# Optimization experiments

Hardware: AMD Instinct MI355X
Metric: run time of the kernel (lower is better)

Reference implementation:

```python
import jax, jax.numpy as jnp
import numpy as np

# Dimensions (source globals scaled to production: r=256 residues, s=128 sequences)
S, R, CM, CZ, C, H = 128, 256, 256, 128, 32, 8
EPS = 1e-5  # torch LayerNorm default


def setup_inputs() -> dict:
    key = jax.random.key(0)
    ks = jax.random.split(key, 14)
    msa = jax.random.normal(ks[0], (S, R, CM), dtype=jnp.float32)
    pair = jax.random.normal(ks[1], (R, R, CZ), dtype=jnp.float32)
    u = lambda k, shape, fan: jax.random.uniform(k, shape, jnp.float32, -1.0 / np.sqrt(fan), 1.0 / np.sqrt(fan))
    return {
        "msa": msa,
        "pair": pair,
        # per-head LayerNorm affine params (stacked over head axis)
        "ln_msa_g": 1.0 + 0.1 * jax.random.normal(ks[2], (H, CM), dtype=jnp.float32),
        "ln_msa_b": 0.1 * jax.random.normal(ks[3], (H, CM), dtype=jnp.float32),
        "ln_pair_g": 1.0 + 0.1 * jax.random.normal(ks[4], (H, CZ), dtype=jnp.float32),
        "ln_pair_b": 0.1 * jax.random.normal(ks[5], (H, CZ), dtype=jnp.float32),
        # per-head projections (torch Linear without bias; stored as (in, out))
        "Wq": u(ks[6], (H, CM, C), CM),
        "Wk": u(ks[7], (H, CM, C), CM),
        "Wv": u(ks[8], (H, CM, C), CM),
        "Wg": u(ks[9], (H, CM, C), CM),
        "Wb": u(ks[10], (H, CZ, S), CZ),  # linear_b: c_z -> s
        # output projection c*H -> c_m (with bias)
        "Wo": u(ks[11], (H * C, CM), H * C),
        "bo": u(ks[12], (CM,), H * C),
    }


def _forward(msa, pair, ln_msa_g, ln_msa_b, ln_pair_g, ln_pair_b, Wq, Wk, Wv, Wg, Wb, Wo, bo):
    # LayerNorm normalization is head-independent; only affine differs per head.
    mu = msa.mean(-1, keepdims=True)
    var = msa.var(-1, keepdims=True)
    nm = (msa - mu) * jax.lax.rsqrt(var + EPS)              # (S, R, CM)
    p = nm[None] * ln_msa_g[:, None, None, :] + ln_msa_b[:, None, None, :]  # (H, S, R, CM)

    q = jnp.einsum("hsrc,hcd->hsrd", p, Wq)                  # (H, S, R, C)
    k = jnp.einsum("hsrc,hcd->hsrd", p, Wk)
    v = jnp.einsum("hsrc,hcd->hsrd", p, Wv)
    g = jax.nn.sigmoid(jnp.einsum("hsrc,hcd->hsrd", p, Wg))

    pmu = pair.mean(-1, keepdims=True)
    pvar = pair.var(-1, keepdims=True)
    npair = (pair - pmu) * jax.lax.rsqrt(pvar + EPS)         # (R, R, CZ)
    pp = npair[None] * ln_pair_g[:, None, None, :] + ln_pair_b[:, None, None, :]  # (H, R, R, CZ)
    bflat = jnp.einsum("hijc,hcs->hijs", pp, Wb)             # (H, R, R, S)
    # Faithful to torch: b = linear_b(flat_pair).view(s, r, r) -- a raw
    # row-major reinterpretation (NOT a transpose).
    b = bflat.reshape(H, S, R, R)

    inv_sqrt_c = np.float32(1.0 / np.sqrt(C))
    scores = (jnp.einsum("hsid,hsjd->hsij", q, k) + b) * inv_sqrt_c  # (H, S, R, R)
    # Source softmax is over dim=-2 (the query/row axis), faithful here.
    a = jax.nn.softmax(scores, axis=-2)
    o = g * jnp.einsum("hsij,hsjd->hsid", a, v)              # (H, S, R, C)

    # concat heads on last dim: (S, R, H*C)
    cat = jnp.transpose(o, (1, 2, 0, 3)).reshape(S, R, H * C)
    return cat @ Wo + bo                                      # (S, R, CM)


def reference(msa, pair, ln_msa_g, ln_msa_b, ln_pair_g, ln_pair_b, Wq, Wk, Wv, Wg, Wb, Wo, bo):
    return _forward(msa, pair, ln_msa_g, ln_msa_b, ln_pair_g, ln_pair_b, Wq, Wk, Wv, Wg, Wb, Wo, bo)
```

## Files before the change

kernel.cpp:

```cpp
#include <hip/hip_runtime.h>
#include <hip/hip_bf16.h>


namespace {
constexpr int S_ = 128, R_ = 256, CM_ = 256, CZ_ = 128, C_ = 32, H_ = 8;
constexpr int SR_ = S_ * R_;
constexpr int RR_ = R_ * R_;
constexpr float EPS_ = 1e-5f;
constexpr float ISC_ = 0.17677669529663687f;

constexpr size_t OFF_MU_M = 0;
constexpr size_t OFF_RS_M = OFF_MU_M + SR_;
constexpr size_t OFF_MU_P = OFF_RS_M + SR_;
constexpr size_t OFF_RS_P = OFF_MU_P + RR_;
constexpr size_t OFF_WC   = OFF_RS_P + RR_;
constexpr size_t OFF_BC   = OFF_WC + (size_t)H_ * CM_ * 128;
constexpr size_t OFF_WBP  = OFF_BC + (size_t)H_ * 128;
constexpr size_t OFF_BBP  = OFF_WBP + (size_t)H_ * CZ_ * 128;
constexpr size_t F32_END  = OFF_BBP + (size_t)H_ * 128;
constexpr size_t BF_BASE  = F32_END * 4;
constexpr size_t QKVG_ELEMS = (size_t)H_ * SR_ * C_;
constexpr size_t CAT_ELEMS  = (size_t)SR_ * CM_;
constexpr size_t WBT_ELEMS  = (size_t)H_ * 128 * 128;
constexpr size_t WOT_ELEMS  = (size_t)256 * 256;
constexpr size_t NEED_BYTES =
    BF_BASE + (4 * QKVG_ELEMS + CAT_ELEMS + WBT_ELEMS + WOT_ELEMS) * 2;
}

typedef unsigned short bf_t;
typedef short s8v __attribute__((ext_vector_type(8)));
typedef float f4v __attribute__((ext_vector_type(4)));

__device__ __forceinline__ unsigned pk2(float lo, float hi) {
  __hip_bfloat162 t = __float22bfloat162_rn(float2{lo, hi});
  return *reinterpret_cast<unsigned*>(&t);
}
__device__ __forceinline__ bf_t pk1(float v) {
  __hip_bfloat16 t = __float2bfloat16(v);
  return *reinterpret_cast<bf_t*>(&t);
}
__device__ __forceinline__ float uplo(unsigned u) { return __uint_as_float(u << 16); }
__device__ __forceinline__ float uphi(unsigned u) { return __uint_as_float(u & 0xffff0000u); }
__device__ __forceinline__ void up8(uint4 u, float* f) {
  f[0] = uplo(u.x); f[1] = uphi(u.x);
  f[2] = uplo(u.y); f[3] = uphi(u.y);
  f[4] = uplo(u.z); f[5] = uphi(u.z);
  f[6] = uplo(u.w); f[7] = uphi(u.w);
}
__device__ __forceinline__ f4v mfma16(s8v a, s8v b, f4v c) {
  return __builtin_amdgcn_mfma_f32_16x16x32_bf16(a, b, c, 0, 0, 0);
}

__global__ void msa_stats_k(const float* __restrict__ msa, float* __restrict__ mu,
                            float* __restrict__ rstd) {
  int row = blockIdx.x * 4 + (threadIdx.x >> 6);
  int lane = threadIdx.x & 63;
  float4 v = reinterpret_cast<const float4*>(msa + (size_t)row * CM_)[lane];
  float s = v.x + v.y + v.z + v.w;
  float s2 = v.x * v.x + v.y * v.y + v.z * v.z + v.w * v.w;
  for (int off = 32; off; off >>= 1) {
    s += __shfl_down(s, off);
    s2 += __shfl_down(s2, off);
  }
  if (lane == 0) {
    float m = s / CM_;
    float var = s2 / CM_ - m * m;
    mu[row] = m;
    rstd[row] = rsqrtf(var + EPS_);
  }
}

__global__ void pair_stats_k(const float* __restrict__ pair, float* __restrict__ mu,
                             float* __restrict__ rstd) {
  int row = blockIdx.x * 4 + (threadIdx.x >> 6);
  int lane = threadIdx.x & 63;
  float2 v = reinterpret_cast<const float2*>(pair + (size_t)row * CZ_)[lane];
  float s = v.x + v.y;
  float s2 = v.x * v.x + v.y * v.y;
  for (int off = 32; off; off >>= 1) {
    s += __shfl_down(s, off);
    s2 += __shfl_down(s2, off);
  }
  if (lane == 0) {
    float m = s / CZ_;
    float var = s2 / CZ_ - m * m;
    mu[row] = m;
    rstd[row] = rsqrtf(var + EPS_);
  }
}

__global__ void prep_weights_k(const float* __restrict__ lng_m, const float* __restrict__ lnb_m,
                               const float* __restrict__ lng_p, const float* __restrict__ lnb_p,
                               const float* __restrict__ Wq, const float* __restrict__ Wk,
                               const float* __restrict__ Wv, const float* __restrict__ Wg,
                               const float* __restrict__ Wb, const float* __restrict__ Wo,
                               bf_t* __restrict__ wct, float* __restrict__ bc,
                               float* __restrict__ Wbp, float* __restrict__ bbp,
                               bf_t* __restrict__ wbt, bf_t* __restrict__ wot) {
  int b = blockIdx.x;
  int t = threadIdx.x;
  if (b < H_) {
    int h = b;
    int m = t >> 5, d = t & 31;
    const float* Wsrc = (m == 0) ? Wq : (m == 1) ? Wk : (m == 2) ? Wv : Wg;
    float scale = (m == 0) ? ISC_ : 1.0f;
    float bias = 0.f;
    for (int c = 0; c < CM_; c++) {
      float w = Wsrc[((size_t)h * CM_ + c) * C_ + d];
      bias += lnb_m[h * CM_ + c] * w;
      wct[((size_t)h * 128 + t) * 256 + c] = pk1(lng_m[h * CM_ + c] * w * scale);
    }
    bc[h * 128 + t] = bias * scale;
  } else if (b < 2 * H_) {
    int h = b - H_;
    float bias = 0.f;
    for (int c = 0; c < CZ_; c++) {
      float w = Wb[((size_t)h * CZ_ + c) * S_ + t];
      bias += lnb_p[h * CZ_ + c] * w;
      Wbp[((size_t)h * CZ_ + c) * 128 + t] = lng_p[h * CZ_ + c] * w * ISC_;
    }
    bbp[h * 128 + t] = bias * ISC_;
    for (int c = 0; c < CZ_; c++)
      wbt[((size_t)h * 128 + t) * 128 + c] = pk1(Wbp[((size_t)h * CZ_ + c) * 128 + t]);
  } else {
    int n = (b - 2 * H_) * 128 + t;
    for (int k = 0; k < 256; k++) wot[(size_t)n * 256 + k] = pk1(Wo[(size_t)k * 256 + n]);
  }
}

__global__ __launch_bounds__(512, 1) void qkvg_mfma_k(
    const float* __restrict__ msa, const float* __restrict__ mu, const float* __restrict__ rstd,
    const bf_t* __restrict__ wct, const float* __restrict__ bc, bf_t* __restrict__ q,
    bf_t* __restrict__ k, bf_t* __restrict__ v, bf_t* __restrict__ g) {
  __shared__ bf_t sm_a[128 * 256];
  __shared__ bf_t sm_w[128 * 256];
  int ib = blockIdx.x;
  int tid = threadIdx.x;
  int w = tid >> 6, l = tid & 63;
  int l15 = l & 15, l4 = l >> 4;
  int iw = w >> 2, jw = w & 3;
  int sr0 = ib * 128;
  int sx7 = l15 & 7;
#pragma unroll
  for (int rep = 0; rep < 8; rep++) {
    int flat = rep * 512 + tid;
    int row = flat >> 5, c = flat & 31;
    int srow = sr0 + row;
    const float4* ps = reinterpret_cast<const float4*>(msa + (size_t)srow * CM_ + c * 8);
    float4 x0 = ps[0], x1 = ps[1];
    float m = mu[srow], rs = rstd[srow];
    uint4 wv;
    wv.x = pk2((x0.x - m) * rs, (x0.y - m) * rs);
    wv.y = pk2((x0.z - m) * rs, (x0.w - m) * rs);
    wv.z = pk2((x1.x - m) * rs, (x1.y - m) * rs);
    wv.w = pk2((x1.z - m) * rs, (x1.w - m) * rs);
    *reinterpret_cast<uint4*>(&sm_a[row * 256 + ((c ^ (row & 7)) << 3)]) = wv;
  }
  for (int h = 0; h < H_; h++) {
    __syncthreads();
#pragma unroll
    for (int rep = 0; rep < 8; rep++) {
      int flat = rep * 512 + tid;
      int row = flat >> 5, c = flat & 31;
      *reinterpret_cast<uint4*>(&sm_w[row * 256 + ((c ^ (row & 7)) << 3)]) =
          *reinterpret_cast<const uint4*>(wct + ((size_t)h * 128 + row) * 256 + c * 8);
    }
    f4v acc[4][2];
#pragma unroll
    for (int jt = 0; jt < 2; jt++) {
      float bb = bc[h * 128 + jw * 32 + jt * 16 + l15];
#pragma unroll
      for (int it = 0; it < 4; it++) acc[it][jt] = f4v{bb, bb, bb, bb};
    }
    __syncthreads();
#pragma unroll
    for (int ks = 0; ks < 8; ks++) {
      int ch = ks * 4 + l4;
      s8v a[4], b[2];
#pragma unroll
      for (int it = 0; it < 4; it++)
        a[it] = *reinterpret_cast<const s8v*>(
            &sm_a[(iw * 64 + it * 16 + l15) * 256 + ((ch ^ sx7) << 3)]);
#pragma unroll
      for (int jt = 0; jt < 2; jt++)
        b[jt] = *reinterpret_cast<const s8v*>(
            &sm_w[(jw * 32 + jt * 16 + l15) * 256 + ((ch ^ sx7) << 3)]);
#pragma unroll
      for (int it = 0; it < 4; it++)
#pragma unroll
        for (int jt = 0; jt < 2; jt++) acc[it][jt] = mfma16(a[it], b[jt], acc[it][jt]);
    }
#pragma unroll
    for (int it = 0; it < 4; it++) {
#pragma unroll
      for (int jt = 0; jt < 2; jt++) {
        int j = jw * 32 + jt * 16 + l15;
        int m_ = j >> 5, d = j & 31;
        bf_t* dst = (m_ == 0) ? q : (m_ == 1) ? k : (m_ == 2) ? v : g;
#pragma unroll
        for (int r = 0; r < 4; r++) {
          int i = iw * 64 + it * 16 + l4 * 4 + r;
          float val = acc[it][jt][r];
          if (m_ == 3) val = 1.f / (1.f + __expf(-val));
          dst[((size_t)h * SR_ + sr0 + i) * C_ + d] = pk1(val);
        }
      }
    }
  }
}

__global__ __launch_bounds__(512, 1) void attn_mfma_k(
    const float* __restrict__ pair, const float* __restrict__ mu_p,
    const float* __restrict__ rs_p, const bf_t* __restrict__ wbt,
    const float* __restrict__ bbp, const bf_t* __restrict__ qg, const bf_t* __restrict__ kg,
    const bf_t* __restrict__ vg, const bf_t* __restrict__ gg, bf_t* __restrict__ cat) {
  __shared__ bf_t sm_pN[256 * 128];
  __shared__ bf_t sm_wt[64 * 128];
  __shared__ bf_t sm_p[256 * 64];
  __shared__ bf_t sm_q[256 * 40];
  __shared__ bf_t sm_k[64 * 40];
  __shared__ bf_t sm_vt[32 * 64];
  __shared__ float sm_redm[4 * 64];
  __shared__ float sm_reds[4 * 64];

  int s = blockIdx.x, h = blockIdx.y;
  int tid = threadIdx.x;
  int w = tid >> 6, l = tid & 63;
  int l15 = l & 15, l4 = l >> 4;
  int iw = w >> 1, jw = w & 1;
  int iw2 = w >> 1, dw = w & 1;
  size_t base = ((size_t)h * SR_ + (size_t)s * R_) * C_;

#pragma unroll
  for (int rep = 0; rep < 2; rep++) {
    int flat = rep * 512 + tid;
    int row = flat >> 2, c = flat & 3;
    *reinterpret_cast<uint4*>(&sm_q[row * 40 + c * 8]) =
        *reinterpret_cast<const uint4*>(qg + base + (size_t)row * C_ + c * 8);
  }

  f4v accO[4];
#pragma unroll
  for (int it = 0; it < 4; it++) accO[it] = f4v{0.f, 0.f, 0.f, 0.f};

  for (int p = 0; p < 2; p++) {
    __syncthreads();
#pragma unroll
    for (int rep = 0; rep < 8; rep++) {
      int flat = rep * 512 + tid;
      int row = flat >> 4, c = flat & 15;
      int gr = (2 * s + (row >> 7)) * 256 + 2 * (row & 127) + p;
      const float4* ps = reinterpret_cast<const float4*>(pair + (size_t)gr * CZ_) + c * 2;
      float4 x0 = ps[0], x1 = ps[1];
      float m = mu_p[gr], rs = rs_p[gr];
      uint4 wv;
      wv.x = pk2((x0.x - m) * rs, (x0.y - m) * rs);
      wv.y = pk2((x0.z - m) * rs, (x0.w - m) * rs);
      wv.z = pk2((x1.x - m) * rs, (x1.y - m) * rs);
      wv.w = pk2((x1.z - m) * rs, (x1.w - m) * rs);
      *reinterpret_cast<uint4*>(&sm_pN[row * 128 + ((c ^ (row & 7)) << 3)]) = wv;
    }
    for (int jh = 0; jh < 2; jh++) {
      int j0 = p * 128 + jh * 64;
      __syncthreads();
#pragma unroll
      for (int rep = 0; rep < 2; rep++) {
        int flat = rep * 512 + tid;
        int row = flat >> 4, c = flat & 15;
        *reinterpret_cast<uint4*>(&sm_wt[row * 128 + ((c ^ (row & 7)) << 3)]) =
            *reinterpret_cast<const uint4*>(wbt + ((size_t)h * 128 + jh * 64 + row) * 128 +
                                            c * 8);
      }
      if (tid < 256) {
        int row = tid >> 2, c = tid & 3;
        *reinterpret_cast<uint4*>(&sm_k[row * 40 + c * 8]) =
            *reinterpret_cast<const uint4*>(kg + base + (size_t)(j0 + row) * C_ + c * 8);
      } else {
        int t2 = tid - 256;
        int j = t2 >> 2, dc = t2 & 3;
        uint4 u = *reinterpret_cast<const uint4*>(vg + base + (size_t)(j0 + j) * C_ + dc * 8);
        unsigned uu[4] = {u.x, u.y, u.z, u.w};
#pragma unroll
        for (int e = 0; e < 8; e++) {
          int d = dc * 8 + e;
          bf_t val = (bf_t)((uu[e >> 1] >> ((e & 1) * 16)) & 0xffff);
          sm_vt[d * 64 + ((((j >> 3) ^ (d & 7)) << 3) + (j & 7))] = val;
        }
      }
      f4v acc[4][2];
      {
        float bb0 = bbp[h * 128 + jh * 64 + jw * 32 + l15];
        float bb1 = bbp[h * 128 + jh * 64 + jw * 32 + 16 + l15];
#pragma unroll
        for (int it = 0; it < 4; it++) {
          acc[it][0] = f4v{bb0, bb0, bb0, bb0};
          acc[it][1] = f4v{bb1, bb1, bb1, bb1};
        }
      }
      __syncthreads();
      int sx7 = l15 & 7;
#pragma unroll
      for (int ks = 0; ks < 4; ks++) {
        int ch = (ks * 4 + l4);
        s8v a[4], b[2];
#pragma unroll
        for (int it = 0; it < 4; it++)
          a[it] = *reinterpret_cast<const s8v*>(
              &sm_pN[(iw * 64 + it * 16 + l15) * 128 + ((ch ^ sx7) << 3)]);
#pragma unroll
        for (int u = 0; u < 2; u++)
          b[u] = *reinterpret_cast<const s8v*>(
              &sm_wt[(jw * 32 + u * 16 + l15) * 128 + ((ch ^ sx7) << 3)]);
#pragma unroll
        for (int it = 0; it < 4; it++) {
          acc[it][0] = mfma16(a[it], b[0], acc[it][0]);
          acc[it][1] = mfma16(a[it], b[1], acc[it][1]);
        }
      }
      {
        s8v qa[4], kb[2];
#pragma unroll
        for (int it = 0; it < 4; it++)
          qa[it] = *reinterpret_cast<const s8v*>(&sm_q[(iw * 64 + it * 16 + l15) * 40 + l4 * 8]);
#pragma unroll
        for (int u = 0; u < 2; u++)
          kb[u] = *reinterpret_cast<const s8v*>(&sm_k[(jw * 32 + u * 16 + l15) * 40 + l4 * 8]);
#pragma unroll
        for (int it = 0; it < 4; it++) {
          acc[it][0] = mfma16(qa[it], kb[0], acc[it][0]);
          acc[it][1] = mfma16(qa[it], kb[1], acc[it][1]);
        }
      }
      float mx[2];
#pragma unroll
      for (int u = 0; u < 2; u++) {
        float m0 = -1e30f;
#pragma unroll
        for (int it = 0; it < 4; it++)
#pragma unroll
          for (int r = 0; r < 4; r++) m0 = fmaxf(m0, acc[it][u][r]);
        m0 = fmaxf(m0, __shfl_xor(m0, 16));
        m0 = fmaxf(m0, __shfl_xor(m0, 32));
        mx[u] = m0;
      }
      if (l < 16) {
        sm_redm[iw * 64 + jw * 32 + l] = mx[0];
        sm_redm[iw * 64 + jw * 32 + 16 + l] = mx[1];
      }
      __syncthreads();
      float M[2], sm[2];
#pragma unroll
      for (int u = 0; u < 2; u++) {
        int jc = jw * 32 + u * 16 + l15;
        float m0 = sm_redm[jc];
        m0 = fmaxf(m0, sm_redm[64 + jc]);
        m0 = fmaxf(m0, sm_redm[128 + jc]);
        m0 = fmaxf(m0, sm_redm[192 + jc]);
        M[u] = m0;
        float s0 = 0.f;
#pragma unroll
        for (int it = 0; it < 4; it++) {
#pragma unroll
          for (int r = 0; r < 4; r++) {
            float e = __expf(acc[it][u][r] - m0);
            acc[it][u][r] = e;
            s0 += e;
          }
        }
        s0 += __shfl_xor(s0, 16);
        s0 += __shfl_xor(s0, 32);
        sm[u] = s0;
      }
      if (l < 16) {
        sm_reds[iw * 64 + jw * 32 + l] = sm[0];
        sm_reds[iw * 64 + jw * 32 + 16 + l] = sm[1];
      }
      __syncthreads();
#pragma unroll
      for (int u = 0; u < 2; u++) {
        int jc = jw * 32 + u * 16 + l15;
        float tot = sm_reds[jc] + sm_reds[64 + jc] + sm_reds[128 + jc] + sm_reds[192 + jc];
        float inv = 1.0f / tot;
#pragma unroll
        for (int it = 0; it < 4; it++) {
#pragma unroll
          for (int r = 0; r < 4; r++) {
            int i = iw * 64 + it * 16 + l4 * 4 + r;
            sm_p[i * 64 + ((((jc >> 3) ^ (i & 7)) << 3) + (jc & 7))] = pk1(acc[it][u][r] * inv);
          }
        }
      }
      __syncthreads();
#pragma unroll
      for (int ks = 0; ks < 2; ks++) {
        int ch = ks * 4 + l4;
        s8v vb = *reinterpret_cast<const s8v*>(
            &sm_vt[(dw * 16 + l15) * 64 + ((ch ^ sx7) << 3)]);
#pragma unroll
        for (int it = 0; it < 4; it++) {
          s8v pa = *reinterpret_cast<const s8v*>(
              &sm_p[(iw2 * 64 + it * 16 + l15) * 64 + ((ch ^ sx7) << 3)]);
          accO[it] = mfma16(pa, vb, accO[it]);
        }
      }
    }
  }
#pragma unroll
  for (int it = 0; it < 4; it++) {
#pragma unroll
    for (int r = 0; r < 4; r++) {
      int i = iw2 * 64 + it * 16 + l4 * 4 + r;
      int d = dw * 16 + l15;
      float gf = uplo((unsigned)gg[base + (size_t)i * C_ + d]);
      cat[((size_t)s * R_ + i) * 256 + h * 32 + d] = pk1(accO[it][r] * gf);
    }
  }
}

__global__ __launch_bounds__(512, 1) void out_mfma_k(const bf_t* __restrict__ cat,
                                                     const bf_t* __restrict__ wot,
                                                     const float* __restrict__ bo,
                                                     float* __restrict__ out) {
  __shared__ bf_t sm_a[128 * 256];
  __shared__ bf_t sm_b[128 * 256];
  int ib = blockIdx.x;
  int tid = threadIdx.x;
  int w = tid >> 6, l = tid & 63;
  int l15 = l & 15, l4 = l >> 4, sx7 = l15 & 7;
  int iw = w >> 2, jw = w & 3;
  int sr0 = ib * 128;
#pragma unroll
  for (int rep = 0; rep < 8; rep++) {
    int flat = rep * 512 + tid;
    int row = flat >> 5, c = flat & 31;
    *reinterpret_cast<uint4*>(&sm_a[row * 256 + ((c ^ (row & 7)) << 3)]) =
        *reinterpret_cast<const uint4*>(cat + (size_t)(sr0 + row) * 256 + c * 8);
  }
  for (int nb = 0; nb < 2; nb++) {
    __syncthreads();
#pragma unroll
    for (int rep = 0; rep < 8; rep++) {
      int flat = rep * 512 + tid;
      int row = flat >> 5, c = flat & 31;
      *reinterpret_cast<uint4*>(&sm_b[row * 256 + ((c ^ (row & 7)) << 3)]) =
          *reinterpret_cast<const uint4*>(wot + (size_t)(nb * 128 + row) * 256 + c * 8);
    }
    f4v acc[4][2];
#pragma unroll
    for (int jt = 0; jt < 2; jt++) {
      float bb = bo[nb * 128 + jw * 32 + jt * 16 + l15];
#pragma unroll
      for (int it = 0; it < 4; it++) acc[it][jt] = f4v{bb, bb, bb, bb};
    }
    __syncthreads();
#pragma unroll
    for (int ks = 0; ks < 8; ks++) {
      int ch = ks * 4 + l4;
      s8v a[4], b[2];
#pragma unroll
      for (int it = 0; it < 4; it++)
        a[it] = *reinterpret_cast<const s8v*>(
            &sm_a[(iw * 64 + it * 16 + l15) * 256 + ((ch ^ sx7) << 3)]);
#pragma unroll
      for (int jt = 0; jt < 2; jt++)
        b[jt] = *reinterpret_cast<const s8v*>(
            &sm_b[(jw * 32 + jt * 16 + l15) * 256 + ((ch ^ sx7) << 3)]);
#pragma unroll
      for (int it = 0; it < 4; it++)
#pragma unroll
        for (int jt = 0; jt < 2; jt++) acc[it][jt] = mfma16(a[it], b[jt], acc[it][jt]);
    }
#pragma unroll
    for (int it = 0; it < 4; it++)
#pragma unroll
      for (int jt = 0; jt < 2; jt++) {
        int n = nb * 128 + jw * 32 + jt * 16 + l15;
#pragma unroll
        for (int r = 0; r < 4; r++) {
          int i = iw * 64 + it * 16 + l4 * 4 + r;
          out[(size_t)(sr0 + i) * 256 + n] = acc[it][jt][r];
        }
      }
  }
}

extern "C" void kernel_launch(void* const* d_in, const int* in_sizes, int n_in, void* d_out,
                              int out_size, void* d_ws, size_t ws_size, hipStream_t stream) {
  if (ws_size < NEED_BYTES) return;

  const float* msa = (const float*)d_in[0];
  const float* pair = (const float*)d_in[1];
  const float* lng_m = (const float*)d_in[2];
  const float* lnb_m = (const float*)d_in[3];
  const float* lng_p = (const float*)d_in[4];
  const float* lnb_p = (const float*)d_in[5];
  const float* Wq = (const float*)d_in[6];
  const float* Wk = (const float*)d_in[7];
  const float* Wv = (const float*)d_in[8];
  const float* Wg = (const float*)d_in[9];
  const float* Wb = (const float*)d_in[10];
  const float* Wo = (const float*)d_in[11];
  const float* bo = (const float*)d_in[12];
  float* out = (float*)d_out;
  float* ws = (float*)d_ws;

  float* mu_m = ws + OFF_MU_M;
  float* rs_m = ws + OFF_RS_M;
  float* mu_p = ws + OFF_MU_P;
  float* rs_p = ws + OFF_RS_P;
  bf_t* wct = (bf_t*)(ws + OFF_WC);
  float* bc = ws + OFF_BC;
  float* Wbp = ws + OFF_WBP;
  float* bbp = ws + OFF_BBP;
  bf_t* qb = (bf_t*)((char*)d_ws + BF_BASE);
  bf_t* kb = qb + QKVG_ELEMS;
  bf_t* vb = kb + QKVG_ELEMS;
  bf_t* gb = vb + QKVG_ELEMS;
  bf_t* cat = gb + QKVG_ELEMS;
  bf_t* wbt = cat + CAT_ELEMS;
  bf_t* wot = wbt + WBT_ELEMS;

  msa_stats_k<<<SR_ / 4, 256, 0, stream>>>(msa, mu_m, rs_m);
  pair_stats_k<<<RR_ / 4, 256, 0, stream>>>(pair, mu_p, rs_p);
  prep_weights_k<<<18, 128, 0, stream>>>(lng_m, lnb_m, lng_p, lnb_p, Wq, Wk, Wv, Wg, Wb, Wo, wct,
                                         bc, Wbp, bbp, wbt, wot);
  qkvg_mfma_k<<<SR_ / 128, 512, 0, stream>>>(msa, mu_m, rs_m, wct, bc, qb, kb, vb, gb);
  attn_mfma_k<<<dim3(S_, H_), 512, 0, stream>>>(pair, mu_p, rs_p, wbt, bbp, qb, kb, vb, gb, cat);
  out_mfma_k<<<SR_ / 128, 512, 0, stream>>>(cat, wot, bo, out);
}
```

Measured before the change: 182.5 us.

## Prenormalize pair to bf16, cut LDS staging, raise occupancy across MFMA kernels

The pair LayerNorm becomes a kernel that writes normalized bf16 rows to workspace, so attention no longer normalizes fp32 pair rows in each block. Attention, QKVG and output kernels drop most shared-memory staging: weights, pair rows, q and k are read straight from global/L2 into MFMA operands. GEMM tiles shrink to 64 rows with launch bounds allowing 4 blocks per CU, which doubles the grid and cuts LDS per block. The aim is higher occupancy and fewer barriers, at the cost of more redundant global/L2 traffic and unswizzled direct loads.

Result: slower. 362.7 us (+98.8%).

```diff
diff --git a/kernel.cpp b/kernel.cpp
--- a/kernel.cpp
+++ b/kernel.cpp
@@ -11,9 +11,7 @@
 
 constexpr size_t OFF_MU_M = 0;
 constexpr size_t OFF_RS_M = OFF_MU_M + SR_;
-constexpr size_t OFF_MU_P = OFF_RS_M + SR_;
-constexpr size_t OFF_RS_P = OFF_MU_P + RR_;
-constexpr size_t OFF_WC   = OFF_RS_P + RR_;
+constexpr size_t OFF_WC   = OFF_RS_M + SR_;
 constexpr size_t OFF_BC   = OFF_WC + (size_t)H_ * CM_ * 128;
 constexpr size_t OFF_WBP  = OFF_BC + (size_t)H_ * 128;
 constexpr size_t OFF_BBP  = OFF_WBP + (size_t)H_ * CZ_ * 128;
@@ -23,8 +21,9 @@
 constexpr size_t CAT_ELEMS  = (size_t)SR_ * CM_;
 constexpr size_t WBT_ELEMS  = (size_t)H_ * 128 * 128;
 constexpr size_t WOT_ELEMS  = (size_t)256 * 256;
+constexpr size_t PAIRN_ELEMS = (size_t)RR_ * 128;
 constexpr size_t NEED_BYTES =
-    BF_BASE + (4 * QKVG_ELEMS + CAT_ELEMS + WBT_ELEMS + WOT_ELEMS) * 2;
+    BF_BASE + (4 * QKVG_ELEMS + CAT_ELEMS + WBT_ELEMS + WOT_ELEMS + PAIRN_ELEMS) * 2;
 }
 
 typedef unsigned short bf_t;
@@ -41,14 +40,11 @@
 }
 __device__ __forceinline__ float uplo(unsigned u) { return __uint_as_float(u << 16); }
 __device__ __forceinline__ float uphi(unsigned u) { return __uint_as_float(u & 0xffff0000u); }
-__device__ __forceinline__ void up8(uint4 u, float* f) {
-  f[0] = uplo(u.x); f[1] = uphi(u.x);
-  f[2] = uplo(u.y); f[3] = uphi(u.y);
-  f[4] = uplo(u.z); f[5] = uphi(u.z);
-  f[6] = uplo(u.w); f[7] = uphi(u.w);
-}
 __device__ __forceinline__ f4v mfma16(s8v a, s8v b, f4v c) {
   return __builtin_amdgcn_mfma_f32_16x16x32_bf16(a, b, c, 0, 0, 0);
+}
+__device__ __forceinline__ s8v ld8(const bf_t* p) {
+  return *reinterpret_cast<const s8v*>(p);
 }
 
 __global__ void msa_stats_k(const float* __restrict__ msa, float* __restrict__ mu,
@@ -70,23 +66,22 @@
   }
 }
 
-__global__ void pair_stats_k(const float* __restrict__ pair, float* __restrict__ mu,
-                             float* __restrict__ rstd) {
-  int row = blockIdx.x * 4 + (threadIdx.x >> 6);
+__global__ __launch_bounds__(512) void pair_norm_k(const float* __restrict__ pair,
+                                                   bf_t* __restrict__ pairN) {
+  int row = blockIdx.x * 8 + (threadIdx.x >> 6);
   int lane = threadIdx.x & 63;
   float2 v = reinterpret_cast<const float2*>(pair + (size_t)row * CZ_)[lane];
   float s = v.x + v.y;
   float s2 = v.x * v.x + v.y * v.y;
   for (int off = 32; off; off >>= 1) {
-    s += __shfl_down(s, off);
-    s2 += __shfl_down(s2, off);
-  }
-  if (lane == 0) {
-    float m = s / CZ_;
-    float var = s2 / CZ_ - m * m;
-    mu[row] = m;
-    rstd[row] = rsqrtf(var + EPS_);
-  }
+    s += __shfl_xor(s, off);
+    s2 += __shfl_xor(s2, off);
+  }
+  float m = s / CZ_;
+  float var = s2 / CZ_ - m * m;
+  float rs = rsqrtf(var + EPS_);
+  reinterpret_cast<unsigned*>(pairN)[(size_t)row * 64 + lane] =
+      pk2((v.x - m) * rs, (v.y - m) * rs);
 }
 
 __global__ void prep_weights_k(const float* __restrict__ lng_m, const float* __restrict__ lnb_m,
@@ -128,21 +123,19 @@
   }
 }
 
-__global__ __launch_bounds__(512, 1) void qkvg_mfma_k(
+__global__ __launch_bounds__(512, 4) void qkvg_mfma_k(
     const float* __restrict__ msa, const float* __restrict__ mu, const float* __restrict__ rstd,
     const bf_t* __restrict__ wct, const float* __restrict__ bc, bf_t* __restrict__ q,
     bf_t* __restrict__ k, bf_t* __restrict__ v, bf_t* __restrict__ g) {
-  __shared__ bf_t sm_a[128 * 256];
-  __shared__ bf_t sm_w[128 * 256];
+  __shared__ bf_t sm_a[64 * 256];
   int ib = blockIdx.x;
   int tid = threadIdx.x;
   int w = tid >> 6, l = tid & 63;
-  int l15 = l & 15, l4 = l >> 4;
+  int l15 = l & 15, l4 = l >> 4, sx7 = l15 & 7;
   int iw = w >> 2, jw = w & 3;
-  int sr0 = ib * 128;
-  int sx7 = l15 & 7;
-#pragma unroll
-  for (int rep = 0; rep < 8; rep++) {
+  int sr0 = ib * 64;
+#pragma unroll
+  for (int rep = 0; rep < 4; rep++) {
     int flat = rep * 512 + tid;
     int row = flat >> 5, c = flat & 31;
     int srow = sr0 + row;
@@ -156,42 +149,32 @@
     wv.w = pk2((x1.z - m) * rs, (x1.w - m) * rs);
     *reinterpret_cast<uint4*>(&sm_a[row * 256 + ((c ^ (row & 7)) << 3)]) = wv;
   }
+  __syncthreads();
   for (int h = 0; h < H_; h++) {
-    __syncthreads();
-#pragma unroll
-    for (int rep = 0; rep < 8; rep++) {
-      int flat = rep * 512 + tid;
-      int row = flat >> 5, c = flat & 31;
-      *reinterpret_cast<uint4*>(&sm_w[row * 256 + ((c ^ (row & 7)) << 3)]) =
-          *reinterpret_cast<const uint4*>(wct + ((size_t)h * 128 + row) * 256 + c * 8);
-    }
-    f4v acc[4][2];
+    f4v acc[2][2];
 #pragma unroll
     for (int jt = 0; jt < 2; jt++) {
       float bb = bc[h * 128 + jw * 32 + jt * 16 + l15];
 #pragma unroll
-      for (int it = 0; it < 4; it++) acc[it][jt] = f4v{bb, bb, bb, bb};
-    }
-    __syncthreads();
+      for (int it = 0; it < 2; it++) acc[it][jt] = f4v{bb, bb, bb, bb};
+    }
 #pragma unroll
     for (int ks = 0; ks < 8; ks++) {
       int ch = ks * 4 + l4;
-      s8v a[4], b[2];
-#pragma unroll
-      for (int it = 0; it < 4; it++)
-        a[it] = *reinterpret_cast<const s8v*>(
-            &sm_a[(iw * 64 + it * 16 + l15) * 256 + ((ch ^ sx7) << 3)]);
+      s8v a[2], b[2];
+#pragma unroll
+      for (int it = 0; it < 2; it++)
+        a[it] = ld8(&sm_a[(iw * 32 + it * 16 + l15) * 256 + ((ch ^ sx7) << 3)]);
 #pragma unroll
       for (int jt = 0; jt < 2; jt++)
-        b[jt] = *reinterpret_cast<const s8v*>(
-            &sm_w[(jw * 32 + jt * 16 + l15) * 256 + ((ch ^ sx7) << 3)]);
-#pragma unroll
-      for (int it = 0; it < 4; it++)
+        b[jt] = ld8(&wct[((size_t)h * 128 + jw * 32 + jt * 16 + l15) * 256 + ch * 8]);
+#pragma unroll
+      for (int it = 0; it < 2; it++)
 #pragma unroll
         for (int jt = 0; jt < 2; jt++) acc[it][jt] = mfma16(a[it], b[jt], acc[it][jt]);
     }
 #pragma unroll
-    for (int it = 0; it < 4; it++) {
+    for (int it = 0; it < 2; it++) {
 #pragma unroll
       for (int jt = 0; jt < 2; jt++) {
         int j = jw * 32 + jt * 16 + l15;
@@ -199,7 +182,7 @@
         bf_t* dst = (m_ == 0) ? q : (m_ == 1) ? k : (m_ == 2) ? v : g;
 #pragma unroll
         for (int r = 0; r < 4; r++) {
-          int i = iw * 64 + it * 16 + l4 * 4 + r;
+          int i = iw * 32 + it * 16 + l4 * 4 + r;
           float val = acc[it][jt][r];
           if (m_ == 3) val = 1.f / (1.f + __expf(-val));
           dst[((size_t)h * SR_ + sr0 + i) * C_ + d] = pk1(val);
@@ -209,16 +192,11 @@
   }
 }
 
-__global__ __launch_bounds__(512, 1) void attn_mfma_k(
-    const float* __restrict__ pair, const float* __restrict__ mu_p,
-    const float* __restrict__ rs_p, const bf_t* __restrict__ wbt,
+__global__ __launch_bounds__(512, 4) void attn_mfma_k(
+    const bf_t* __restrict__ pairN, const bf_t* __restrict__ wbt,
     const float* __restrict__ bbp, const bf_t* __restrict__ qg, const bf_t* __restrict__ kg,
     const bf_t* __restrict__ vg, const bf_t* __restrict__ gg, bf_t* __restrict__ cat) {
-  __shared__ bf_t sm_pN[256 * 128];
-  __shared__ bf_t sm_wt[64 * 128];
   __shared__ bf_t sm_p[256 * 64];
-  __shared__ bf_t sm_q[256 * 40];
-  __shared__ bf_t sm_k[64 * 40];
   __shared__ bf_t sm_vt[32 * 64];
   __shared__ float sm_redm[4 * 64];
   __shared__ float sm_reds[4 * 64];
@@ -226,184 +204,142 @@
   int s = blockIdx.x, h = blockIdx.y;
   int tid = threadIdx.x;
   int w = tid >> 6, l = tid & 63;
-  int l15 = l & 15, l4 = l >> 4;
+  int l15 = l & 15, l4 = l >> 4, sx7 = l15 & 7;
   int iw = w >> 1, jw = w & 1;
   int iw2 = w >> 1, dw = w & 1;
   size_t base = ((size_t)h * SR_ + (size_t)s * R_) * C_;
-
-#pragma unroll
-  for (int rep = 0; rep < 2; rep++) {
-    int flat = rep * 512 + tid;
-    int row = flat >> 2, c = flat & 3;
-    *reinterpret_cast<uint4*>(&sm_q[row * 40 + c * 8]) =
-        *reinterpret_cast<const uint4*>(qg + base + (size_t)row * C_ + c * 8);
-  }
+  const bf_t* wbh = wbt + (size_t)h * 128 * 128;
 
   f4v accO[4];
 #pragma unroll
   for (int it = 0; it < 4; it++) accO[it] = f4v{0.f, 0.f, 0.f, 0.f};
 
-  for (int p = 0; p < 2; p++) {
+  for (int pass = 0; pass < 4; pass++) {
+    int p = pass >> 1, jh = pass & 1;
+    int j0 = p * 128 + jh * 64;
+    if (tid >= 256) {
+      int t2 = tid - 256;
+      int j = t2 >> 2, dc = t2 & 3;
+      uint4 u = *reinterpret_cast<const uint4*>(vg + base + (size_t)(j0 + j) * C_ + dc * 8);
+      unsigned uu[4] = {u.x, u.y, u.z, u.w};
+#pragma unroll
+      for (int e = 0; e < 8; e++) {
+        int d = dc * 8 + e;
+        bf_t val = (bf_t)((uu[e >> 1] >> ((e & 1) * 16)) & 0xffff);
+        sm_vt[d * 64 + ((((j >> 3) ^ (d & 7)) << 3) + (j & 7))] = val;
+      }
+    }
+    f4v acc[4][2];
+    {
+      float bb0 = bbp[h * 128 + jh * 64 + jw * 32 + l15];
+      float bb1 = bbp[h * 128 + jh * 64 + jw * 32 + 16 + l15];
+#pragma unroll
+      for (int it = 0; it < 4; it++) {
+        acc[it][0] = f4v{bb0, bb0, bb0, bb0};
+        acc[it][1] = f4v{bb1, bb1, bb1, bb1};
+      }
+    }
+#pragma unroll
+    for (int ks = 0; ks < 4; ks++) {
+      int ch = ks * 4 + l4;
+      s8v a[4], b[2];
+#pragma unroll
+      for (int it = 0; it < 4; it++) {
+        int i = iw * 64 + it * 16 + l15;
+        size_t gr = (size_t)(2 * s + (i >> 7)) * 256 + 2 * (i & 127) + p;
+        a[it] = ld8(&pairN[gr * 128 + ch * 8]);
+      }
+#pragma unroll
+      for (int u = 0; u < 2; u++)
+        b[u] = ld8(&wbh[(size_t)(jh * 64 + jw * 32 + u * 16 + l15) * 128 + ch * 8]);
+#pragma unroll
+      for (int it = 0; it < 4; it++) {
+        acc[it][0] = mfma16(a[it], b[0], acc[it][0]);
+        acc[it][1] = mfma16(a[it], b[1], acc[it][1]);
+      }
+    }
+    {
+      s8v qa[4], kb[2];
+#pragma unroll
+      for (int it = 0; it < 4; it++)
+        qa[it] = ld8(&qg[base + (size_t)(iw * 64 + it * 16 + l15) * C_ + l4 * 8]);
+#pragma unroll
+      for (int u = 0; u < 2; u++)
+        kb[u] = ld8(&kg[base + (size_t)(j0 + jw * 32 + u * 16 + l15) * C_ + l4 * 8]);
+#pragma unroll
+      for (int it = 0; it < 4; it++) {
+        acc[it][0] = mfma16(qa[it], kb[0], acc[it][0]);
+        acc[it][1] = mfma16(qa[it], kb[1], acc[it][1]);
+      }
+    }
+    float mx[2];
+#pragma unroll
+    for (int u = 0; u < 2; u++) {
+      float m0 = -1e30f;
+#pragma unroll
+      for (int it = 0; it < 4; it++)
+#pragma unroll
+        for (int r = 0; r < 4; r++) m0 = fmaxf(m0, acc[it][u][r]);
+      m0 = fmaxf(m0, __shfl_xor(m0, 16));
+      m0 = fmaxf(m0, __shfl_xor(m0, 32));
+      mx[u] = m0;
+    }
+    if (l < 16) {
+      sm_redm[iw * 64 + jw * 32 + l] = mx[0];
+      sm_redm[iw * 64 + jw * 32 + 16 + l] = mx[1];
+    }
     __syncthreads();
-#pragma unroll
-    for (int rep = 0; rep < 8; rep++) {
-      int flat = rep * 512 + tid;
-      int row = flat >> 4, c = flat & 15;
-      int gr = (2 * s + (row >> 7)) * 256 + 2 * (row & 127) + p;
-      const float4* ps = reinterpret_cast<const float4*>(pair + (size_t)gr * CZ_) + c * 2;
-      float4 x0 = ps[0], x1 = ps[1];
-      float m = mu_p[gr], rs = rs_p[gr];
-      uint4 wv;
-      wv.x = pk2((x0.x - m) * rs, (x0.y - m) * rs);
-      wv.y = pk2((x0.z - m) * rs, (x0.w - m) * rs);
-      wv.z = pk2((x1.x - m) * rs, (x1.y - m) * rs);
-      wv.w = pk2((x1.z - m) * rs, (x1.w - m) * rs);
-      *reinterpret_cast<uint4*>(&sm_pN[row * 128 + ((c ^ (row & 7)) << 3)]) = wv;
-    }
-    for (int jh = 0; jh < 2; jh++) {
-      int j0 = p * 128 + jh * 64;
-      __syncthreads();
-#pragma unroll
-      for (int rep = 0; rep < 2; rep++) {
-        int flat = rep * 512 + tid;
-        int row = flat >> 4, c = flat & 15;
-        *reinterpret_cast<uint4*>(&sm_wt[row * 128 + ((c ^ (row & 7)) << 3)]) =
-            *reinterpret_cast<const uint4*>(wbt + ((size_t)h * 128 + jh * 64 + row) * 128 +
-                                            c * 8);
-      }
-      if (tid < 256) {
-        int row = tid >> 2, c = tid & 3;
-        *reinterpret_cast<uint4*>(&sm_k[row * 40 + c * 8]) =
-            *reinterpret_cast<const uint4*>(kg + base + (size_t)(j0 + row) * C_ + c * 8);
-      } else {
-        int t2 = tid - 256;
-        int j = t2 >> 2, dc = t2 & 3;
-        uint4 u = *reinterpret_cast<const uint4*>(vg + base + (size_t)(j0 + j) * C_ + dc * 8);
-        unsigned uu[4] = {u.x, u.y, u.z, u.w};
-#pragma unroll
-        for (int e = 0; e < 8; e++) {
-          int d = dc * 8 + e;
-          bf_t val = (bf_t)((uu[e >> 1] >> ((e & 1) * 16)) & 0xffff);
-          sm_vt[d * 64 + ((((j >> 3) ^ (d & 7)) << 3) + (j & 7))] = val;
+    float sm[2];
+#pragma unroll
+    for (int u = 0; u < 2; u++) {
+      int jc = jw * 32 + u * 16 + l15;
+      float m0 = fmaxf(fmaxf(sm_redm[jc], sm_redm[64 + jc]),
+                       fmaxf(sm_redm[128 + jc], sm_redm[192 + jc]));
+      float s0 = 0.f;
+#pragma unroll
+      for (int it = 0; it < 4; it++) {
+#pragma unroll
+        for (int r = 0; r < 4; r++) {
+          float e = __expf(acc[it][u][r] - m0);
+          acc[it][u][r] = e;
+          s0 += e;
         }
       }
-      f4v acc[4][2];
-      {
-        float bb0 = bbp[h * 128 + jh * 64 + jw * 32 + l15];
-        float bb1 = bbp[h * 128 + jh * 64 + jw * 32 + 16 + l15];
-#pragma unroll
-        for (int it = 0; it < 4; it++) {
-          acc[it][0] = f4v{bb0, bb0, bb0, bb0};
-          acc[it][1] = f4v{bb1, bb1, bb1, bb1};
+      s0 += __shfl_xor(s0, 16);
+      s0 += __shfl_xor(s0, 32);
+      sm[u] = s0;
+    }
+    if (l < 16) {
+      sm_reds[iw * 64 + jw * 32 + l] = sm[0];
+      sm_reds[iw * 64 + jw * 32 + 16 + l] = sm[1];
+    }
+    __syncthreads();
+#pragma unroll
+    for (int u = 0; u < 2; u++) {
+      int jc = jw * 32 + u * 16 + l15;
+      float tot = sm_reds[jc] + sm_reds[64 + jc] + sm_reds[128 + jc] + sm_reds[192 + jc];
+      float inv = 1.0f / tot;
+#pragma unroll
+      for (int it = 0; it < 4; it++) {
+#pragma unroll
+        for (int r = 0; r < 4; r++) {
+          int i = iw * 64 + it * 16 + l4 * 4 + r;
+          sm_p[i * 64 + ((((jc >> 3) ^ (i & 7)) << 3) + (jc & 7))] = pk1(acc[it][u][r] * inv);
         }
       }
-      __syncthreads();
-      int sx7 = l15 & 7;
-#pragma unroll
-      for (int ks = 0; ks < 4; ks++) {
-        int ch = (ks * 4 + l4);
-        s8v a[4], b[2];
-#pragma unroll
-        for (int it = 0; it < 4; it++)
-          a[it] = *reinterpret_cast<const s8v*>(
-              &sm_pN[(iw * 64 + it * 16 + l15) * 128 + ((ch ^ sx7) << 3)]);
-#pragma unroll
-        for (int u = 0; u < 2; u++)
-          b[u] = *reinterpret_cast<const s8v*>(
-              &sm_wt[(jw * 32 + u * 16 + l15) * 128 + ((ch ^ sx7) << 3)]);
-#pragma unroll
-        for (int it = 0; it < 4; it++) {
-          acc[it][0] = mfma16(a[it], b[0], acc[it][0]);
-          acc[it][1] = mfma16(a[it], b[1], acc[it][1]);
-        }
-      }
-      {
-        s8v qa[4], kb[2];
-#pragma unroll
-        for (int it = 0; it < 4; it++)
-          qa[it] = *reinterpret_cast<const s8v*>(&sm_q[(iw * 64 + it * 16 + l15) * 40 + l4 * 8]);
-#pragma unroll
-        for (int u = 0; u < 2; u++)
-          kb[u] = *reinterpret_cast<const s8v*>(&sm_k[(jw * 32 + u * 16 + l15) * 40 + l4 * 8]);
-#pragma unroll
-        for (int it = 0; it < 4; it++) {
-          acc[it][0] = mfma16(qa[it], kb[0], acc[it][0]);
-          acc[it][1] = mfma16(qa[it], kb[1], acc[it][1]);
-        }
-      }
-      float mx[2];
-#pragma unroll
-      for (int u = 0; u < 2; u++) {
-        float m0 = -1e30f;
-#pragma unroll
-        for (int it = 0; it < 4; it++)
-#pragma unroll
-          for (int r = 0; r < 4; r++) m0 = fmaxf(m0, acc[it][u][r]);
-        m0 = fmaxf(m0, __shfl_xor(m0, 16));
-        m0 = fmaxf(m0, __shfl_xor(m0, 32));
-        mx[u] = m0;
-      }
-      if (l < 16) {
-        sm_redm[iw * 64 + jw * 32 + l] = mx[0];
-        sm_redm[iw * 64 + jw * 32 + 16 + l] = mx[1];
-      }
-      __syncthreads();
-      float M[2], sm[2];
-#pragma unroll
-      for (int u = 0; u < 2; u++) {
-        int jc = jw * 32 + u * 16 + l15;
-        float m0 = sm_redm[jc];
-        m0 = fmaxf(m0, sm_redm[64 + jc]);
-        m0 = fmaxf(m0, sm_redm[128 + jc]);
-        m0 = fmaxf(m0, sm_redm[192 + jc]);
-        M[u] = m0;
-        float s0 = 0.f;
-#pragma unroll
-        for (int it = 0; it < 4; it++) {
-#pragma unroll
-          for (int r = 0; r < 4; r++) {
-            float e = __expf(acc[it][u][r] - m0);
-            acc[it][u][r] = e;
-            s0 += e;
-          }
-        }
-        s0 += __shfl_xor(s0, 16);
-        s0 += __shfl_xor(s0, 32);
-        sm[u] = s0;
-      }
-      if (l < 16) {
-        sm_reds[iw * 64 + jw * 32 + l] = sm[0];
-        sm_reds[iw * 64 + jw * 32 + 16 + l] = sm[1];
-      }
-      __syncthreads();
-#pragma unroll
-      for (int u = 0; u < 2; u++) {
-        int jc = jw * 32 + u * 16 + l15;
-        float tot = sm_reds[jc] + sm_reds[64 + jc] + sm_reds[128 + jc] + sm_reds[192 + jc];
-        float inv = 1.0f / tot;
-#pragma unroll
-        for (int it = 0; it < 4; it++) {
-#pragma unroll
-          for (int r = 0; r < 4; r++) {
-            int i = iw * 64 + it * 16 + l4 * 4 + r;
-            sm_p[i * 64 + ((((jc >> 3) ^ (i & 7)) << 3) + (jc & 7))] = pk1(acc[it][u][r] * inv);
-          }
-        }
-      }
-      __syncthreads();
-#pragma unroll
-      for (int ks = 0; ks < 2; ks++) {
-        int ch = ks * 4 + l4;
-        s8v vb = *reinterpret_cast<const s8v*>(
-            &sm_vt[(dw * 16 + l15) * 64 + ((ch ^ sx7) << 3)]);
-#pragma unroll
-        for (int it = 0; it < 4; it++) {
-          s8v pa = *reinterpret_cast<const s8v*>(
-              &sm_p[(iw2 * 64 + it * 16 + l15) * 64 + ((ch ^ sx7) << 3)]);
-          accO[it] = mfma16(pa, vb, accO[it]);
-        }
-      }
-    }
+    }
+    __syncthreads();
+#pragma unroll
+    for (int ks = 0; ks < 2; ks++) {
+      int ch = ks * 4 + l4;
+      s8v vb = ld8(&sm_vt[(dw * 16 + l15) * 64 + ((ch ^ sx7) << 3)]);
+#pragma unroll
+      for (int it = 0; it < 4; it++) {
+        s8v pa = ld8(&sm_p[(iw2 * 64 + it * 16 + l15) * 64 + ((ch ^ sx7) << 3)]);
+        accO[it] = mfma16(pa, vb, accO[it]);
+      }
+    }
+    __syncthreads();
   }
 #pragma unroll
   for (int it = 0; it < 4; it++) {
@@ -417,67 +353,56 @@
   }
 }
 
-__global__ __launch_bounds__(512, 1) void out_mfma_k(const bf_t* __restrict__ cat,
+__global__ __launch_bounds__(512, 4) void out_mfma_k(const bf_t* __restrict__ cat,
                                                      const bf_t* __restrict__ wot,
                                                      const float* __restrict__ bo,
                                                      float* __restrict__ out) {
-  __shared__ bf_t sm_a[128 * 256];
-  __shared__ bf_t sm_b[128 * 256];
+  __shared__ bf_t sm_a[64 * 256];
   int ib = blockIdx.x;
   int tid = threadIdx.x;
   int w = tid >> 6, l = tid & 63;
   int l15 = l & 15, l4 = l >> 4, sx7 = l15 & 7;
   int iw = w >> 2, jw = w & 3;
-  int sr0 = ib * 128;
-#pragma unroll
-  for (int rep = 0; rep < 8; rep++) {
+  int sr0 = ib * 64;
+#pragma unroll
+  for (int rep = 0; rep < 4; rep++) {
     int flat = rep * 512 + tid;
     int row = flat >> 5, c = flat & 31;
     *reinterpret_cast<uint4*>(&sm_a[row * 256 + ((c ^ (row & 7)) << 3)]) =
         *reinterpret_cast<const uint4*>(cat + (size_t)(sr0 + row) * 256 + c * 8);
   }
+  __syncthreads();
   for (int nb = 0; nb < 2; nb++) {
-    __syncthreads();
-#pragma unroll
-    for (int rep = 0; rep < 8; rep++) {
-      int flat = rep * 512 + tid;
-      int row = flat >> 5, c = flat & 31;
-      *reinterpret_cast<uint4*>(&sm_b[row * 256 + ((c ^ (row & 7)) << 3)]) =
-          *reinterpret_cast<const uint4*>(wot + (size_t)(nb * 128 + row) * 256 + c * 8);
-    }
-    f4v acc[4][2];
+    f4v acc[2][2];
 #pragma unroll
     for (int jt = 0; jt < 2; jt++) {
       float bb = bo[nb * 128 + jw * 32 + jt * 16 + l15];
 #pragma unroll
-      for (int it = 0; it < 4; it++) acc[it][jt] = f4v{bb, bb, bb, bb};
-    }
-    __syncthreads();
+      for (int it = 0; it < 2; it++) acc[it][jt] = f4v{bb, bb, bb, bb};
+    }
 #pragma unroll
     for (int ks = 0; ks < 8; ks++) {
       int ch = ks * 4 + l4;
-      s8v a[4], b[2];
-#pragma unroll
-      for (int it = 0; it < 4; it++)
-        a[it] = *reinterpret_cast<const s8v*>(
-            &sm_a[(iw * 64 + it * 16 + l15) * 256 + ((ch ^ sx7) << 3)]);
+      s8v a[2], b[2];
+#pragma unroll
+      for (int it = 0; it < 2; it++)
+        a[it] = ld8(&sm_a[(iw * 32 + it * 16 + l15) * 256 + ((ch ^ sx7) << 3)]);
 #pragma unroll
       for (int jt = 0; jt < 2; jt++)
-        b[jt] = *reinterpret_cast<const s8v*>(
-            &sm_b[(jw * 32 + jt * 16 + l15) * 256 + ((ch ^ sx7) << 3)]);
-#pragma unroll
-      for (int it = 0; it < 4; it++)
+        b[jt] = ld8(&wot[(size_t)(nb * 128 + jw * 32 + jt * 16 + l15) * 256 + ch * 8]);
+#pragma unroll
+      for (int it = 0; it < 2; it++)
 #pragma unroll
         for (int jt = 0; jt < 2; jt++) acc[it][jt] = mfma16(a[it], b[jt], acc[it][jt]);
     }
 #pragma unroll
-    for (int it = 0; it < 4; it++)
+    for (int it = 0; it < 2; it++)
 #pragma unroll
       for (int jt = 0; jt < 2; jt++) {
         int n = nb * 128 + jw * 32 + jt * 16 + l15;
 #pragma unroll
         for (int r = 0; r < 4; r++) {
-          int i = iw * 64 + it * 16 + l4 * 4 + r;
+          int i = iw * 32 + it * 16 + l4 * 4 + r;
           out[(size_t)(sr0 + i) * 256 + n] = acc[it][jt][r];
         }
       }
@@ -506,8 +431,6 @@
 
   float* mu_m = ws + OFF_MU_M;
   float* rs_m = ws + OFF_RS_M;
-  float* mu_p = ws + OFF_MU_P;
-  float* rs_p = ws + OFF_RS_P;
   bf_t* wct = (bf_t*)(ws + OFF_WC);
   float* bc = ws + OFF_BC;
   float* Wbp = ws + OFF_WBP;
@@ -519,12 +442,13 @@
   bf_t* cat = gb + QKVG_ELEMS;
   bf_t* wbt = cat + CAT_ELEMS;
   bf_t* wot = wbt + WBT_ELEMS;
+  bf_t* pairN = wot + WOT_ELEMS;
 
   msa_stats_k<<<SR_ / 4, 256, 0, stream>>>(msa, mu_m, rs_m);
-  pair_stats_k<<<RR_ / 4, 256, 0, stream>>>(pair, mu_p, rs_p);
+  pair_norm_k<<<RR_ / 8, 512, 0, stream>>>(pair, pairN);
   prep_weights_k<<<18, 128, 0, stream>>>(lng_m, lnb_m, lng_p, lnb_p, Wq, Wk, Wv, Wg, Wb, Wo, wct,
                                          bc, Wbp, bbp, wbt, wot);
-  qkvg_mfma_k<<<SR_ / 128, 512, 0, stream>>>(msa, mu_m, rs_m, wct, bc, qb, kb, vb, gb);
-  attn_mfma_k<<<dim3(S_, H_), 512, 0, stream>>>(pair, mu_p, rs_p, wbt, bbp, qb, kb, vb, gb, cat);
-  out_mfma_k<<<SR_ / 128, 512, 0, stream>>>(cat, wot, bo, out);
-}
+  qkvg_mfma_k<<<SR_ / 64, 512, 0, stream>>>(msa, mu_m, rs_m, wct, bc, qb, kb, vb, gb);
+  attn_mfma_k<<<dim3(S_, H_), 512, 0, stream>>>(pairN, wbt, bbp, qb, kb, vb, gb, cat);
+  out_mfma_k<<<SR_ / 64, 512, 0, stream>>>(cat, wot, bo, out);
+}
```
